# Kernel optimization log

Hardware: AMD Instinct MI355X
Metric: run time of the kernel (lower is better)

The kernel has to match this reference:

```python
import jax, jax.numpy as jnp
import numpy as np

B, N, C = 4, 1029, 1024
H = 16           # num_heads
L = 8            # num_blocks
DH = C // H      # head_dim = 64
HID = 4 * C      # mlp hidden
SCALE = DH ** -0.5
EPS = 1e-6


def _ln(x, w, b):
    mu = jnp.mean(x, axis=-1, keepdims=True)
    var = jnp.var(x, axis=-1, keepdims=True)
    return (x - mu) * jax.lax.rsqrt(var + EPS) * w + b


def setup_inputs() -> dict:
    key = jax.random.key(0)
    ks = jax.random.split(key, 16)
    s = 0.02
    return {
        "x": jax.random.normal(ks[0], (B, N, C), dtype=jnp.float32),
        "ln1_w": jnp.ones((L, C), jnp.float32),
        "ln1_b": jnp.zeros((L, C), jnp.float32),
        "qkv_w": jax.random.normal(ks[1], (L, 3 * C, C), jnp.float32) * s,
        "qkv_b": jnp.zeros((L, 3 * C), jnp.float32),
        "proj_w": jax.random.normal(ks[2], (L, C, C), jnp.float32) * s,
        "proj_b": jnp.zeros((L, C), jnp.float32),
        "ln2_w": jnp.ones((L, C), jnp.float32),
        "ln2_b": jnp.zeros((L, C), jnp.float32),
        "fc1_w": jax.random.normal(ks[3], (L, HID, C), jnp.float32) * s,
        "fc1_b": jnp.zeros((L, HID), jnp.float32),
        "fc2_w": jax.random.normal(ks[4], (L, C, HID), jnp.float32) * s,
        "fc2_b": jnp.zeros((L, C), jnp.float32),
        "norm_w": jnp.ones((C,), jnp.float32),
        "norm_b": jnp.zeros((C,), jnp.float32),
    }


def _block(x, p):
    ln1_w, ln1_b, qkv_w, qkv_b, proj_w, proj_b, ln2_w, ln2_b, fc1_w, fc1_b, fc2_w, fc2_b = p
    # --- attention (manual fp32 QK^T / softmax / AV, as in Attention.forward) ---
    h = _ln(x, ln1_w, ln1_b)
    qkv = h @ qkv_w.T + qkv_b                        # [B,N,3C]
    qkv = qkv.reshape(B, N, 3, H, DH).transpose(2, 0, 3, 1, 4)  # [3,B,H,N,DH]
    q, k, v = qkv[0], qkv[1], qkv[2]
    attn = jnp.einsum("bhnd,bhmd->bhnm", q.astype(jnp.float32), k.astype(jnp.float32)) * SCALE
    # original subtracts row max before softmax; jax.nn.softmax is the same stable math
    attn = jax.nn.softmax(attn, axis=-1).astype(v.dtype)
    o = jnp.einsum("bhnm,bhmd->bhnd", attn, v)       # [B,H,N,DH]
    o = o.transpose(0, 2, 1, 3).reshape(B, N, C)
    x = x + (o @ proj_w.T + proj_b)
    # --- MLP (exact GELU, as nn.GELU default) ---
    h = _ln(x, ln2_w, ln2_b)
    h = jax.nn.gelu(h @ fc1_w.T + fc1_b, approximate=False)
    x = x + (h @ fc2_w.T + fc2_b)
    return x


def reference(x, ln1_w, ln1_b, qkv_w, qkv_b, proj_w, proj_b, ln2_w, ln2_b,
              fc1_w, fc1_b, fc2_w, fc2_b, norm_w, norm_b):
    params = (ln1_w, ln1_b, qkv_w, qkv_b, proj_w, proj_b, ln2_w, ln2_b,
              fc1_w, fc1_b, fc2_w, fc2_b)

    def body(h, p):
        return _block(h, p), None

    x, _ = jax.lax.scan(body, x, params)
    return _ln(x, norm_w, norm_b)
```

## Files before the change

### kernel.cpp

```cpp
#include <hip/hip_runtime.h>
#include <cstdint>
#include <cstddef>

#define B_    4
#define N_TOK 1029
#define C_    1024
#define H_    16
#define L_    8
#define HID_  4096
#define M_TOK (B_*N_TOK)
#define MP2_  4352
#define PROWS 4224
#define KVB_  128
#define KVT2_ 9
#define KPAD_ 1152

typedef float f32x4 __attribute__((ext_vector_type(4)));
typedef short bf16x8 __attribute__((ext_vector_type(8)));

__device__ __forceinline__ uint16_t f2bf(float f) {
  uint32_t u = __float_as_uint(f);
  u += 0x7fffu + ((u >> 16) & 1u);
  return (uint16_t)(u >> 16);
}

__device__ __forceinline__ void async_copy16(const uint16_t* src, uint16_t* lds_dst) {
  __builtin_amdgcn_global_load_lds(
      (const __attribute__((address_space(1))) void*)src,
      (__attribute__((address_space(3))) void*)lds_dst, 16, 0, 0);
}

__device__ __forceinline__ int swz16(int row, int byte_in_row) {
  return row * 128 + (byte_in_row ^ ((row & 7) << 4));
}

__global__ __launch_bounds__(256)
void cvt_f32_bf16(const float* __restrict__ in, uint16_t* __restrict__ out, int n4) {
  int i = blockIdx.x * 256 + threadIdx.x;
  if (i < n4) {
    float4 v = reinterpret_cast<const float4*>(in)[i];
    uint64_t pk = (uint64_t)f2bf(v.x) | ((uint64_t)f2bf(v.y) << 16)
                | ((uint64_t)f2bf(v.z) << 32) | ((uint64_t)f2bf(v.w) << 48);
    reinterpret_cast<uint64_t*>(out)[i] = pk;
  }
}

template<int OUTMODE>
__global__ __launch_bounds__(256)
void ln_fwd(const float* __restrict__ x, const float* __restrict__ w,
            const float* __restrict__ b, void* __restrict__ outp) {
  const int row = blockIdx.x;
  const int tid = threadIdx.x;
  const float4 v = reinterpret_cast<const float4*>(x + (size_t)row * C_)[tid];
  float s  = v.x + v.y + v.z + v.w;
  float s2 = v.x*v.x + v.y*v.y + v.z*v.z + v.w*v.w;
  #pragma unroll
  for (int d = 1; d < 64; d <<= 1) {
    s  += __shfl_xor(s, d);
    s2 += __shfl_xor(s2, d);
  }
  __shared__ float red[8];
  const int wv = tid >> 6;
  if ((tid & 63) == 0) { red[wv] = s; red[wv + 4] = s2; }
  __syncthreads();
  s  = red[0] + red[1] + red[2] + red[3];
  s2 = red[4] + red[5] + red[6] + red[7];
  const float mu = s * (1.0f / C_);
  const float rs = rsqrtf(fmaxf(s2 * (1.0f / C_) - mu * mu, 0.0f) + 1e-6f);
  const float4 wv4 = reinterpret_cast<const float4*>(w)[tid];
  const float4 bv4 = reinterpret_cast<const float4*>(b)[tid];
  const float o0 = (v.x - mu) * rs * wv4.x + bv4.x;
  const float o1 = (v.y - mu) * rs * wv4.y + bv4.y;
  const float o2 = (v.z - mu) * rs * wv4.z + bv4.z;
  const float o3 = (v.w - mu) * rs * wv4.w + bv4.w;
  uint64_t pk = (uint64_t)f2bf(o0) | ((uint64_t)f2bf(o1) << 16)
              | ((uint64_t)f2bf(o2) << 32) | ((uint64_t)f2bf(o3) << 48);
  reinterpret_cast<uint64_t*>((uint16_t*)outp + (size_t)row * C_)[tid] = pk;
}

template<int KCH, int OUT>
__global__ __launch_bounds__(256)
void reduce_ln(const float* __restrict__ pbuf, const float* __restrict__ bias,
               float* __restrict__ xbuf, const float* __restrict__ lw,
               const float* __restrict__ lb, void* __restrict__ outp) {
  const int m = blockIdx.x;
  const int c4 = threadIdx.x;
  float4 s = reinterpret_cast<const float4*>(bias)[c4];
  #pragma unroll
  for (int kc = 0; kc < KCH; ++kc) {
    const float4 pv = reinterpret_cast<const float4*>(pbuf + ((size_t)kc * PROWS + m) * C_)[c4];
    s.x += pv.x; s.y += pv.y; s.z += pv.z; s.w += pv.w;
  }
  float4 x = reinterpret_cast<float4*>(xbuf + (size_t)m * C_)[c4];
  x.x += s.x; x.y += s.y; x.z += s.z; x.w += s.w;
  reinterpret_cast<float4*>(xbuf + (size_t)m * C_)[c4] = x;
  float ss  = x.x + x.y + x.z + x.w;
  float ss2 = x.x*x.x + x.y*x.y + x.z*x.z + x.w*x.w;
  #pragma unroll
  for (int d = 1; d < 64; d <<= 1) {
    ss  += __shfl_xor(ss, d);
    ss2 += __shfl_xor(ss2, d);
  }
  __shared__ float red[8];
  const int wv = c4 >> 6;
  if ((c4 & 63) == 0) { red[wv] = ss; red[wv + 4] = ss2; }
  __syncthreads();
  ss  = red[0] + red[1] + red[2] + red[3];
  ss2 = red[4] + red[5] + red[6] + red[7];
  const float mu = ss * (1.0f / C_);
  const float rs = rsqrtf(fmaxf(ss2 * (1.0f / C_) - mu * mu, 0.0f) + 1e-6f);
  const float4 wv4 = reinterpret_cast<const float4*>(lw)[c4];
  const float4 bv4 = reinterpret_cast<const float4*>(lb)[c4];
  const float o0 = (x.x - mu) * rs * wv4.x + bv4.x;
  const float o1 = (x.y - mu) * rs * wv4.y + bv4.y;
  const float o2 = (x.z - mu) * rs * wv4.z + bv4.z;
  const float o3 = (x.w - mu) * rs * wv4.w + bv4.w;
  if (OUT == 0) {
    uint64_t pk = (uint64_t)f2bf(o0) | ((uint64_t)f2bf(o1) << 16)
                | ((uint64_t)f2bf(o2) << 32) | ((uint64_t)f2bf(o3) << 48);
    reinterpret_cast<uint64_t*>((uint16_t*)outp + (size_t)m * C_)[c4] = pk;
  } else {
    float4 o; o.x = o0; o.y = o1; o.z = o2; o.w = o3;
    reinterpret_cast<float4*>((float*)outp + (size_t)m * C_)[c4] = o;
  }
}

template<int EPI>
__device__ __forceinline__ void epi_store(int m, int col, float v, int Nn, int kc,
    const float* bias, uint16_t* outb, float* pbuf,
    uint16_t* Qp, uint16_t* Kp, uint16_t* VTp) {
  if (EPI == 3) {
    pbuf[((size_t)kc * PROWS + m) * C_ + col] = v;
  } else if (EPI == 1) {
    const float vb = v + bias[col];
    const float u = -1.5957691216f * (vb + 0.044715f * vb * vb * vb);
    const float g = vb * __builtin_amdgcn_rcpf(1.0f + __expf(u));
    outb[(size_t)m * Nn + col] = f2bf(g);
  } else {
    if (m < M_TOK) {
      const float vb = v + bias[col];
      const int which = col >> 10;
      const int h = (col >> 6) & 15;
      const int d = col & 63;
      const int b = m / N_TOK;
      const int key = m - b * N_TOK;
      const int bh = b * 16 + h;
      if (which == 0)      Qp[((size_t)bh * KPAD_ + key) * 64 + d] = f2bf(vb * 0.125f);
      else if (which == 1) Kp[((size_t)bh * KPAD_ + key) * 64 + d] = f2bf(vb);
      else                 VTp[((size_t)bh * 64 + d) * KPAD_ + key] = f2bf(vb);
    }
  }
}

template<int EPI, int SPLIT>
__global__ __launch_bounds__(512, 4)
void gemm_s(const uint16_t* __restrict__ A, const uint16_t* __restrict__ W,
            const float* __restrict__ bias, uint16_t* __restrict__ outb,
            float* __restrict__ pbuf, int Nn, int Ktot,
            uint16_t* __restrict__ Qp, uint16_t* __restrict__ Kp,
            uint16_t* __restrict__ VTp) {
  const int nbn = Nn >> 8;
  const int KC = Ktot / SPLIT;
  const int nwg = (int)gridDim.x;
  const int q8 = nwg >> 3, r8 = nwg & 7;
  const int xcd = (int)blockIdx.x & 7, pos = (int)blockIdx.x >> 3;
  const int wgid = (xcd < r8 ? xcd * (q8 + 1) : r8 * (q8 + 1) + (xcd - r8) * q8) + pos;
  const int kc  = wgid / (33 * nbn);
  const int rem = wgid % (33 * nbn);
  const int bm = rem % 33, bn = rem / 33;

  const int tid = (int)threadIdx.x;
  const int l = tid & 63, w = tid >> 6;
  const int l15 = l & 15, l4 = l >> 4;
  const int wr = w >> 2, wc = w & 3;

  __shared__ char lds[49152];

  const uint16_t* Ag = A + (size_t)bm * 128 * Ktot + (size_t)kc * KC;
  const uint16_t* Wg = W + (size_t)bn * 256 * Ktot + (size_t)kc * KC;

  const int srow = tid >> 3;
  const int schunk = (tid & 7) ^ (srow & 7);
  const int csel0 = ((l4) ^ (l15 & 7)) << 4;
  const int csel1 = ((4 + l4) ^ (l15 & 7)) << 4;

  bf16x8 rA0, rA1, rB0, rB1, rB2, rB3;
  auto gload = [&](int toff) {
    rA0 = *(const bf16x8*)(Ag + (size_t)(srow)      * Ktot + toff + schunk * 8);
    rA1 = *(const bf16x8*)(Ag + (size_t)(64 + srow) * Ktot + toff + schunk * 8);
    rB0 = *(const bf16x8*)(Wg + (size_t)(srow)       * Ktot + toff + schunk * 8);
    rB1 = *(const bf16x8*)(Wg + (size_t)(64 + srow)  * Ktot + toff + schunk * 8);
    rB2 = *(const bf16x8*)(Wg + (size_t)(128 + srow) * Ktot + toff + schunk * 8);
    rB3 = *(const bf16x8*)(Wg + (size_t)(192 + srow) * Ktot + toff + schunk * 8);
  };

  f32x4 acc[4][4] = {};
  const int nt = KC >> 6;
  gload(0);
  for (int t = 0; t < nt; ++t) {
    __syncthreads();
    *(bf16x8*)(lds +         tid * 16) = rA0;
    *(bf16x8*)(lds +  8192 + tid * 16) = rA1;
    *(bf16x8*)(lds + 16384 + tid * 16) = rB0;
    *(bf16x8*)(lds + 24576 + tid * 16) = rB1;
    *(bf16x8*)(lds + 32768 + tid * 16) = rB2;
    *(bf16x8*)(lds + 40960 + tid * 16) = rB3;
    __syncthreads();
    if (t + 1 < nt) gload((t + 1) * 64);
    __builtin_amdgcn_sched_barrier(0);
    #pragma unroll
    for (int kk = 0; kk < 2; ++kk) {
      const int cs = kk ? csel1 : csel0;
      bf16x8 afr[4], bfr[4];
      #pragma unroll
      for (int f = 0; f < 4; ++f)
        afr[f] = *(const bf16x8*)(lds + (wr * 64 + f * 16 + l15) * 128 + cs);
      #pragma unroll
      for (int nf = 0; nf < 4; ++nf)
        bfr[nf] = *(const bf16x8*)(lds + 16384 + (wc * 64 + nf * 16 + l15) * 128 + cs);
      #pragma unroll
      for (int f = 0; f < 4; ++f)
        #pragma unroll
        for (int nf = 0; nf < 4; ++nf)
          acc[f][nf] = __builtin_amdgcn_mfma_f32_16x16x32_bf16(afr[f], bfr[nf], acc[f][nf], 0, 0, 0);
    }
  }

  #pragma unroll
  for (int nf = 0; nf < 4; ++nf) {
    const int col = bn * 256 + wc * 64 + nf * 16 + l15;
    #pragma unroll
    for (int mf = 0; mf < 4; ++mf) {
      const int mb = bm * 128 + wr * 64 + mf * 16 + l4 * 4;
      #pragma unroll
      for (int r = 0; r < 4; ++r)
        epi_store<EPI>(mb + r, col, acc[mf][nf][r], Nn, kc, bias, outb, pbuf,
                       Qp, Kp, VTp);
    }
  }
}

__global__ __launch_bounds__(256, 4)
void attn_fwd(const uint16_t* __restrict__ Qp, const uint16_t* __restrict__ Kp,
              const uint16_t* __restrict__ VTp, uint16_t* __restrict__ ob) {
  __shared__ uint16_t Ksm_[KVB_ * 64];
  __shared__ uint16_t Vsm_[64 * KVB_];

  const int tid = (int)threadIdx.x;
  const int l = tid & 63, w = tid >> 6;
  const int l15 = l & 15, l4 = l >> 4;
  const int bh = (int)blockIdx.x;
  const int qt = (int)blockIdx.y;

  const uint16_t* Kb = Kp + (size_t)bh * KPAD_ * 64;
  const uint16_t* Vb = VTp + (size_t)bh * 64 * KPAD_;

  bf16x8 qf[2];
  {
    const int qrow = qt * 64 + w * 16 + l15;
    const uint16_t* qbase = Qp + ((size_t)bh * KPAD_ + qrow) * 64;
    qf[0] = *(const bf16x8*)(qbase + l4 * 8);
    qf[1] = *(const bf16x8*)(qbase + 32 + l4 * 8);
  }

  float mrow = -1e30f, lrow = 0.0f;
  f32x4 oacc[4] = {};

  const int krow_s = tid >> 3;
  const int kslot_s = (tid & 7) ^ (krow_s & 7);
  const int vd_s = tid >> 4;
  const int vslot_s = (tid & 15) ^ (vd_s & 15);

  uint16_t* Pls = Ksm_ + w * 2048;
  const int swz_q = l15 & 7;

  for (int kt = 0; kt < KVT2_; ++kt) {
    const int key0 = kt * KVB_;
    __syncthreads();
    #pragma unroll
    for (int it = 0; it < 4; ++it) {
      const int row = it * 32 + krow_s;
      async_copy16(Kb + (size_t)(key0 + row) * 64 + kslot_s * 8,
                   Ksm_ + it * 2048 + tid * 8);
    }
    #pragma unroll
    for (int it = 0; it < 4; ++it) {
      const int d = it * 16 + vd_s;
      async_copy16(Vb + (size_t)d * KPAD_ + key0 + vslot_s * 8,
                   Vsm_ + it * 2048 + tid * 8);
    }
    __syncthreads();

    f32x4 s[8];
    #pragma unroll
    for (int kf = 0; kf < 8; ++kf) s[kf] = f32x4{0.f, 0.f, 0.f, 0.f};
    #pragma unroll
    for (int kk = 0; kk < 2; ++kk) {
      #pragma unroll
      for (int kf = 0; kf < 8; ++kf) {
        const bf16x8 kfrag = *(const bf16x8*)((const char*)Ksm_ + swz16(kf * 16 + l15, kk * 64 + l4 * 16));
        s[kf] = __builtin_amdgcn_mfma_f32_16x16x32_bf16(kfrag, qf[kk], s[kf], 0, 0, 0);
      }
    }
    __syncthreads();

    if (kt == KVT2_ - 1) {
      #pragma unroll
      for (int kf = 0; kf < 8; ++kf)
        #pragma unroll
        for (int r = 0; r < 4; ++r)
          if (key0 + kf * 16 + l4 * 4 + r >= N_TOK) s[kf][r] = -1e30f;
    }
    float pmx = s[0][0];
    #pragma unroll
    for (int kf = 0; kf < 8; ++kf)
      #pragma unroll
      for (int r = 0; r < 4; ++r) pmx = fmaxf(pmx, s[kf][r]);
    pmx = fmaxf(pmx, __shfl_xor(pmx, 16));
    pmx = fmaxf(pmx, __shfl_xor(pmx, 32));
    if (!__all(pmx - mrow <= 8.0f)) {
      const float mi = fmaxf(mrow, pmx);
      const float sc = __expf(mrow - mi);
      mrow = mi;
      lrow *= sc;
      #pragma unroll
      for (int df = 0; df < 4; ++df)
        #pragma unroll
        for (int r = 0; r < 4; ++r) oacc[df][r] *= sc;
    }
    float psum = 0.0f;
    #pragma unroll
    for (int kf = 0; kf < 8; ++kf) {
      const float p0 = __expf(s[kf][0] - mrow);
      const float p1 = __expf(s[kf][1] - mrow);
      const float p2 = __expf(s[kf][2] - mrow);
      const float p3 = __expf(s[kf][3] - mrow);
      psum += (p0 + p1) + (p2 + p3);
      const uint64_t pk = (uint64_t)f2bf(p0) | ((uint64_t)f2bf(p1) << 16)
                        | ((uint64_t)f2bf(p2) << 32) | ((uint64_t)f2bf(p3) << 48);
      const int gr = (kf * 2 + (l4 >> 1)) ^ swz_q;
      *(uint64_t*)(Pls + l15 * 128 + gr * 8 + (l4 & 1) * 4) = pk;
    }
    psum += __shfl_xor(psum, 16);
    psum += __shfl_xor(psum, 32);
    lrow += psum;
    #pragma unroll
    for (int kk = 0; kk < 4; ++kk) {
      const bf16x8 pf = *(const bf16x8*)(Pls + l15 * 128 + (((kk * 4 + l4) ^ swz_q) * 8));
      #pragma unroll
      for (int df = 0; df < 4; ++df) {
        const int d = df * 16 + l15;
        const bf16x8 vfrag = *(const bf16x8*)(Vsm_ + d * KVB_ + (((kk * 4 + l4) ^ (d & 15)) * 8));
        oacc[df] = __builtin_amdgcn_mfma_f32_16x16x32_bf16(vfrag, pf, oacc[df], 0, 0, 0);
      }
    }
  }

  const int q = qt * 64 + w * 16 + l15;
  if (q < N_TOK) {
    const float inv = 1.0f / lrow;
    const int m = (bh >> 4) * N_TOK + q;
    const int hbase = (bh & 15) * 64;
    #pragma unroll
    for (int df = 0; df < 4; ++df)
      #pragma unroll
      for (int r = 0; r < 4; ++r) {
        const int c = hbase + df * 16 + l4 * 4 + r;
        ob[(size_t)m * C_ + c] = f2bf(oacc[df][r] * inv);
      }
  }
}

extern "C" void kernel_launch(void* const* d_in, const int* in_sizes, int n_in,
                              void* d_out, int out_size, void* d_ws, size_t ws_size,
                              hipStream_t stream) {
  const float* x_in   = (const float*)d_in[0];
  const float* ln1_w  = (const float*)d_in[1];
  const float* ln1_b  = (const float*)d_in[2];
  const float* qkv_w  = (const float*)d_in[3];
  const float* qkv_b  = (const float*)d_in[4];
  const float* proj_w = (const float*)d_in[5];
  const float* proj_b = (const float*)d_in[6];
  const float* ln2_w  = (const float*)d_in[7];
  const float* ln2_b  = (const float*)d_in[8];
  const float* fc1_w  = (const float*)d_in[9];
  const float* fc1_b  = (const float*)d_in[10];
  const float* fc2_w  = (const float*)d_in[11];
  const float* fc2_b  = (const float*)d_in[12];
  const float* norm_w = (const float*)d_in[13];
  const float* norm_b = (const float*)d_in[14];

  char* p = (char*)d_ws;
  float*    xbuf = (float*)p;     p += (size_t)MP2_ * C_ * 4;
  uint16_t* hbuf = (uint16_t*)p;  p += (size_t)MP2_ * C_ * 2;
  uint16_t* big  = (uint16_t*)p;  p += (size_t)MP2_ * HID_ * 2;
  uint16_t* wq   = (uint16_t*)p;  p += (size_t)L_ * 3 * C_ * C_ * 2;
  uint16_t* wp   = (uint16_t*)p;  p += (size_t)L_ * C_ * C_ * 2;
  uint16_t* w1   = (uint16_t*)p;  p += (size_t)L_ * HID_ * C_ * 2;
  uint16_t* w2   = (uint16_t*)p;  p += (size_t)L_ * C_ * HID_ * 2;
  uint16_t* qp   = (uint16_t*)p;  p += (size_t)64 * KPAD_ * 64 * 2;
  uint16_t* kp   = (uint16_t*)p;  p += (size_t)64 * KPAD_ * 64 * 2;
  uint16_t* vtp  = (uint16_t*)p;  p += (size_t)64 * 64 * KPAD_ * 2;
  float*    pbuf = (float*)p;     p += (size_t)4 * PROWS * C_ * 4;
  if ((size_t)(p - (char*)d_ws) > ws_size) return;

  hipMemcpyAsync(xbuf, x_in, (size_t)M_TOK * C_ * sizeof(float),
                 hipMemcpyDeviceToDevice, stream);

  auto cvt = [&](const float* src, uint16_t* dst, size_t n) {
    const int n4 = (int)(n / 4);
    cvt_f32_bf16<<<dim3((n4 + 255) / 256), dim3(256), 0, stream>>>(src, dst, n4);
  };
  cvt(qkv_w,  wq, (size_t)L_ * 3 * C_ * C_);
  cvt(proj_w, wp, (size_t)L_ * C_ * C_);
  cvt(fc1_w,  w1, (size_t)L_ * HID_ * C_);
  cvt(fc2_w,  w2, (size_t)L_ * C_ * HID_);

  ln_fwd<0><<<dim3(M_TOK), dim3(256), 0, stream>>>(xbuf, ln1_w, ln1_b, hbuf);

  for (int lyr = 0; lyr < L_; ++lyr) {
    gemm_s<0, 1><<<dim3(396), dim3(512), 0, stream>>>(
        hbuf, wq + (size_t)lyr * 3 * C_ * C_, qkv_b + (size_t)lyr * 3 * C_,
        nullptr, nullptr, 3 * C_, C_, qp, kp, vtp);
    attn_fwd<<<dim3(64, 17), dim3(256), 0, stream>>>(qp, kp, vtp, hbuf);
    gemm_s<3, 2><<<dim3(264), dim3(512), 0, stream>>>(
        hbuf, wp + (size_t)lyr * C_ * C_, nullptr, nullptr, pbuf, C_, C_,
        nullptr, nullptr, nullptr);
    reduce_ln<2, 0><<<dim3(M_TOK), dim3(256), 0, stream>>>(
        pbuf, proj_b + (size_t)lyr * C_, xbuf,
        ln2_w + (size_t)lyr * C_, ln2_b + (size_t)lyr * C_, hbuf);
    gemm_s<1, 1><<<dim3(528), dim3(512), 0, stream>>>(
        hbuf, w1 + (size_t)lyr * HID_ * C_, fc1_b + (size_t)lyr * HID_,
        big, nullptr, HID_, C_, nullptr, nullptr, nullptr);
    gemm_s<3, 4><<<dim3(528), dim3(512), 0, stream>>>(
        big, w2 + (size_t)lyr * C_ * HID_, nullptr, nullptr, pbuf, C_, HID_,
        nullptr, nullptr, nullptr);
    if (lyr < L_ - 1) {
      reduce_ln<4, 0><<<dim3(M_TOK), dim3(256), 0, stream>>>(
          pbuf, fc2_b + (size_t)lyr * C_, xbuf,
          ln1_w + (size_t)(lyr + 1) * C_, ln1_b + (size_t)(lyr + 1) * C_, hbuf);
    } else {
      reduce_ln<4, 1><<<dim3(M_TOK), dim3(256), 0, stream>>>(
          pbuf, fc2_b + (size_t)lyr * C_, xbuf, norm_w, norm_b, d_out);
    }
  }
}
```

Baseline: 2.466 ms.

## Store split-K partials in bf16 and enlarge attention tiles to 128 queries

Split-K GEMM partial sums are now written to and read from the workspace as bf16 instead of fp32, which halves the partial-buffer traffic between the projection/fc2 GEMMs and the reduce+LayerNorm kernels. The attention kernel moves to 512 threads covering 128 query rows per block, so each K/V tile is loaded once for twice as many queries. It also gets its own P scratch in LDS, which removes one barrier. The bf16 partials lose precision in the residual accumulation, and the larger attention block raises LDS use and register pressure.

```diff
diff --git a/kernel.cpp b/kernel.cpp
--- a/kernel.cpp
+++ b/kernel.cpp
@@ -13,6 +13,7 @@
 #define PROWS 4224
 #define KVB_  128
 #define KVT2_ 9
+#define QT2_  9
 #define KPAD_ 1152
 
 typedef float f32x4 __attribute__((ext_vector_type(4)));
@@ -22,6 +23,10 @@
   uint32_t u = __float_as_uint(f);
   u += 0x7fffu + ((u >> 16) & 1u);
   return (uint16_t)(u >> 16);
+}
+
+__device__ __forceinline__ float bf2f(uint16_t h) {
+  return __uint_as_float((uint32_t)h << 16);
 }
 
 __device__ __forceinline__ void async_copy16(const uint16_t* src, uint16_t* lds_dst) {
@@ -80,7 +85,7 @@
 
 template<int KCH, int OUT>
 __global__ __launch_bounds__(256)
-void reduce_ln(const float* __restrict__ pbuf, const float* __restrict__ bias,
+void reduce_ln(const uint16_t* __restrict__ pbuf, const float* __restrict__ bias,
                float* __restrict__ xbuf, const float* __restrict__ lw,
                const float* __restrict__ lb, void* __restrict__ outp) {
   const int m = blockIdx.x;
@@ -88,8 +93,11 @@
   float4 s = reinterpret_cast<const float4*>(bias)[c4];
   #pragma unroll
   for (int kc = 0; kc < KCH; ++kc) {
-    const float4 pv = reinterpret_cast<const float4*>(pbuf + ((size_t)kc * PROWS + m) * C_)[c4];
-    s.x += pv.x; s.y += pv.y; s.z += pv.z; s.w += pv.w;
+    const uint64_t pv = *(const uint64_t*)(pbuf + ((size_t)kc * PROWS + m) * C_ + c4 * 4);
+    s.x += bf2f((uint16_t)pv);
+    s.y += bf2f((uint16_t)(pv >> 16));
+    s.z += bf2f((uint16_t)(pv >> 32));
+    s.w += bf2f((uint16_t)(pv >> 48));
   }
   float4 x = reinterpret_cast<float4*>(xbuf + (size_t)m * C_)[c4];
   x.x += s.x; x.y += s.y; x.z += s.z; x.w += s.w;
@@ -127,10 +135,10 @@
 
 template<int EPI>
 __device__ __forceinline__ void epi_store(int m, int col, float v, int Nn, int kc,
-    const float* bias, uint16_t* outb, float* pbuf,
+    const float* bias, uint16_t* outb,
     uint16_t* Qp, uint16_t* Kp, uint16_t* VTp) {
   if (EPI == 3) {
-    pbuf[((size_t)kc * PROWS + m) * C_ + col] = v;
+    outb[((size_t)kc * PROWS + m) * C_ + col] = f2bf(v);
   } else if (EPI == 1) {
     const float vb = v + bias[col];
     const float u = -1.5957691216f * (vb + 0.044715f * vb * vb * vb);
@@ -156,7 +164,7 @@
 __global__ __launch_bounds__(512, 4)
 void gemm_s(const uint16_t* __restrict__ A, const uint16_t* __restrict__ W,
             const float* __restrict__ bias, uint16_t* __restrict__ outb,
-            float* __restrict__ pbuf, int Nn, int Ktot,
+            int Nn, int Ktot,
             uint16_t* __restrict__ Qp, uint16_t* __restrict__ Kp,
             uint16_t* __restrict__ VTp) {
   const int nbn = Nn >> 8;
@@ -234,17 +242,18 @@
       const int mb = bm * 128 + wr * 64 + mf * 16 + l4 * 4;
       #pragma unroll
       for (int r = 0; r < 4; ++r)
-        epi_store<EPI>(mb + r, col, acc[mf][nf][r], Nn, kc, bias, outb, pbuf,
+        epi_store<EPI>(mb + r, col, acc[mf][nf][r], Nn, kc, bias, outb,
                        Qp, Kp, VTp);
     }
   }
 }
 
-__global__ __launch_bounds__(256, 4)
+__global__ __launch_bounds__(512, 4)
 void attn_fwd(const uint16_t* __restrict__ Qp, const uint16_t* __restrict__ Kp,
               const uint16_t* __restrict__ VTp, uint16_t* __restrict__ ob) {
   __shared__ uint16_t Ksm_[KVB_ * 64];
   __shared__ uint16_t Vsm_[64 * KVB_];
+  __shared__ uint16_t Psm_[8][16 * 128];
 
   const int tid = (int)threadIdx.x;
   const int l = tid & 63, w = tid >> 6;
@@ -257,7 +266,7 @@
 
   bf16x8 qf[2];
   {
-    const int qrow = qt * 64 + w * 16 + l15;
+    const int qrow = qt * 128 + w * 16 + l15;
     const uint16_t* qbase = Qp + ((size_t)bh * KPAD_ + qrow) * 64;
     qf[0] = *(const bf16x8*)(qbase + l4 * 8);
     qf[1] = *(const bf16x8*)(qbase + 32 + l4 * 8);
@@ -267,27 +276,27 @@
   f32x4 oacc[4] = {};
 
   const int krow_s = tid >> 3;
-  const int kslot_s = (tid & 7) ^ (krow_s & 7);
+  const int kslot_s = tid & 7;
   const int vd_s = tid >> 4;
-  const int vslot_s = (tid & 15) ^ (vd_s & 15);
-
-  uint16_t* Pls = Ksm_ + w * 2048;
+  const int vslot_s = tid & 15;
+
+  uint16_t* Pls = &Psm_[w][0];
   const int swz_q = l15 & 7;
 
   for (int kt = 0; kt < KVT2_; ++kt) {
     const int key0 = kt * KVB_;
     __syncthreads();
     #pragma unroll
-    for (int it = 0; it < 4; ++it) {
-      const int row = it * 32 + krow_s;
-      async_copy16(Kb + (size_t)(key0 + row) * 64 + kslot_s * 8,
-                   Ksm_ + it * 2048 + tid * 8);
-    }
-    #pragma unroll
-    for (int it = 0; it < 4; ++it) {
-      const int d = it * 16 + vd_s;
-      async_copy16(Vb + (size_t)d * KPAD_ + key0 + vslot_s * 8,
-                   Vsm_ + it * 2048 + tid * 8);
+    for (int it = 0; it < 2; ++it) {
+      const int row = it * 64 + krow_s;
+      async_copy16(Kb + (size_t)(key0 + row) * 64 + (kslot_s ^ (row & 7)) * 8,
+                   Ksm_ + it * 4096 + tid * 8);
+    }
+    #pragma unroll
+    for (int it = 0; it < 2; ++it) {
+      const int d = it * 32 + vd_s;
+      async_copy16(Vb + (size_t)d * KPAD_ + key0 + (vslot_s ^ (d & 15)) * 8,
+                   Vsm_ + it * 4096 + tid * 8);
     }
     __syncthreads();
 
@@ -302,8 +311,6 @@
         s[kf] = __builtin_amdgcn_mfma_f32_16x16x32_bf16(kfrag, qf[kk], s[kf], 0, 0, 0);
       }
     }
-    __syncthreads();
-
     if (kt == KVT2_ - 1) {
       #pragma unroll
       for (int kf = 0; kf < 8; ++kf)
@@ -356,7 +363,7 @@
     }
   }
 
-  const int q = qt * 64 + w * 16 + l15;
+  const int q = qt * 128 + w * 16 + l15;
   if (q < N_TOK) {
     const float inv = 1.0f / lrow;
     const int m = (bh >> 4) * N_TOK + q;
@@ -401,7 +408,7 @@
   uint16_t* qp   = (uint16_t*)p;  p += (size_t)64 * KPAD_ * 64 * 2;
   uint16_t* kp   = (uint16_t*)p;  p += (size_t)64 * KPAD_ * 64 * 2;
   uint16_t* vtp  = (uint16_t*)p;  p += (size_t)64 * 64 * KPAD_ * 2;
-  float*    pbuf = (float*)p;     p += (size_t)4 * PROWS * C_ * 4;
+  uint16_t* pbuf = (uint16_t*)p;  p += (size_t)4 * PROWS * C_ * 2;
   if ((size_t)(p - (char*)d_ws) > ws_size) return;
 
   hipMemcpyAsync(xbuf, x_in, (size_t)M_TOK * C_ * sizeof(float),
@@ -421,19 +428,19 @@
   for (int lyr = 0; lyr < L_; ++lyr) {
     gemm_s<0, 1><<<dim3(396), dim3(512), 0, stream>>>(
         hbuf, wq + (size_t)lyr * 3 * C_ * C_, qkv_b + (size_t)lyr * 3 * C_,
-        nullptr, nullptr, 3 * C_, C_, qp, kp, vtp);
-    attn_fwd<<<dim3(64, 17), dim3(256), 0, stream>>>(qp, kp, vtp, hbuf);
+        nullptr, 3 * C_, C_, qp, kp, vtp);
+    attn_fwd<<<dim3(64, QT2_), dim3(512), 0, stream>>>(qp, kp, vtp, hbuf);
     gemm_s<3, 2><<<dim3(264), dim3(512), 0, stream>>>(
-        hbuf, wp + (size_t)lyr * C_ * C_, nullptr, nullptr, pbuf, C_, C_,
+        hbuf, wp + (size_t)lyr * C_ * C_, nullptr, pbuf, C_, C_,
         nullptr, nullptr, nullptr);
     reduce_ln<2, 0><<<dim3(M_TOK), dim3(256), 0, stream>>>(
         pbuf, proj_b + (size_t)lyr * C_, xbuf,
         ln2_w + (size_t)lyr * C_, ln2_b + (size_t)lyr * C_, hbuf);
     gemm_s<1, 1><<<dim3(528), dim3(512), 0, stream>>>(
         hbuf, w1 + (size_t)lyr * HID_ * C_, fc1_b + (size_t)lyr * HID_,
-        big, nullptr, HID_, C_, nullptr, nullptr, nullptr);
+        big, HID_, C_, nullptr, nullptr, nullptr);
     gemm_s<3, 4><<<dim3(528), dim3(512), 0, stream>>>(
-        big, w2 + (size_t)lyr * C_ * HID_, nullptr, nullptr, pbuf, C_, HID_,
+        big, w2 + (size_t)lyr * C_ * HID_, nullptr, pbuf, C_, HID_,
         nullptr, nullptr, nullptr);
     if (lyr < L_ - 1) {
       reduce_ln<4, 0><<<dim3(M_TOK), dim3(256), 0, stream>>>(
```

After: 2.392 ms. -3.0%, faster.
